# Optimization experiments

Measured on AMD Instinct MI355X. Metric: run time of the kernel, lower is better.

Reference implementation:

```python
import jax, jax.numpy as jnp
import numpy as np
from jax import lax

SEQ, B, IN, H, NLAYERS, OUT_LEN, OUT_SIZE = 80, 32768, 2, 10, 2, 20, 2


def _lstm_layer(x, h0, c0, Wih, Whh, bih, bhh):
    """PyTorch-convention LSTM layer. x: [T,B,F], h0/c0: [B,H]. Returns [T,B,H]."""
    b = bih + bhh  # [4H]

    def step(carry, xt):
        h, c = carry
        gates = xt @ Wih.T + h @ Whh.T + b  # [B,4H], gate order i,f,g,o
        i, f, g, o = jnp.split(gates, 4, axis=-1)
        i = jax.nn.sigmoid(i)
        f = jax.nn.sigmoid(f)
        g = jnp.tanh(g)
        o = jax.nn.sigmoid(o)
        c = f * c + i * g
        h = o * jnp.tanh(c)
        return (h, c), h

    (_, _), ys = lax.scan(step, (h0, c0), x)
    return ys


def setup_inputs() -> dict:
    key = jax.random.key(0)
    ks = jax.random.split(key, 16)
    s = 1.0 / np.sqrt(H)  # torch default init scale
    u = lambda k, shp: jax.random.uniform(k, shp, jnp.float32, -s, s)
    inp = {
        "x": jax.random.normal(ks[0], (SEQ, B, IN), jnp.float32),
        "h0": jnp.zeros((NLAYERS, B, H), jnp.float32),
        "c0": jnp.zeros((NLAYERS, B, H), jnp.float32),
        # layer 0 LSTM params
        "Wih0": u(ks[1], (4 * H, IN)),
        "Whh0": u(ks[2], (4 * H, H)),
        "bih0": u(ks[3], (4 * H,)),
        "bhh0": u(ks[4], (4 * H,)),
        # layer 1 LSTM params
        "Wih1": u(ks[5], (4 * H, H)),
        "Whh1": u(ks[6], (4 * H, H)),
        "bih1": u(ks[7], (4 * H,)),
        "bhh1": u(ks[8], (4 * H,)),
        # MLP head: Linear(800 -> 10), Sigmoid, Linear(10 -> 40)
        "W1": jax.random.uniform(ks[9], (H, SEQ * H), jnp.float32, -1 / np.sqrt(SEQ * H), 1 / np.sqrt(SEQ * H)),
        "b1": jax.random.uniform(ks[10], (H,), jnp.float32, -1 / np.sqrt(SEQ * H), 1 / np.sqrt(SEQ * H)),
        "W2": u(ks[11], (OUT_LEN * OUT_SIZE, H)),
        "b2": u(ks[12], (OUT_LEN * OUT_SIZE,)),
    }
    return inp


def reference(x, h0, c0, Wih0, Whh0, bih0, bhh0, Wih1, Whh1, bih1, bhh1, W1, b1, W2, b2):
    y0 = _lstm_layer(x, h0[0], c0[0], Wih0, Whh0, bih0, bhh0)   # [T,B,H]
    y1 = _lstm_layer(y0, h0[1], c0[1], Wih1, Whh1, bih1, bhh1)  # [T,B,H]
    out = jnp.tanh(y1)
    out = out.reshape(B, -1)  # faithful to torch .view(batch, -1) on [T,B,H]
    out = jax.nn.sigmoid(out @ W1.T + b1)
    out = out @ W2.T + b2  # [B, OUT_LEN*OUT_SIZE]
    return out.reshape(OUT_LEN, B, OUT_SIZE)
```

## Files before the change

kernel.cpp:

```cpp
#include <hip/hip_runtime.h>
#include <hip/hip_fp16.h>

#define SEQ   80
#define BATCH 32768
#define HID   10

typedef unsigned int uint;
typedef unsigned short ushort;
typedef _Float16 f16;
typedef __attribute__((ext_vector_type(8))) _Float16 f16x8;
typedef __attribute__((ext_vector_type(2))) _Float16 f16x2;
typedef __attribute__((ext_vector_type(4))) float f32x4;

#define SIG_SCALE  (-1.44269504f)
#define TANH_SCALE (-2.88539008f)

__device__ __forceinline__ float fast_rcp(float x)  { return __builtin_amdgcn_rcpf(x); }
__device__ __forceinline__ float fast_exp2(float x) { return __builtin_amdgcn_exp2f(x); }
__device__ __forceinline__ float sigp(float a)  { return fast_rcp(1.0f + fast_exp2(a)); }
__device__ __forceinline__ float tanhp(float a) { return 2.0f * fast_rcp(1.0f + fast_exp2(a)) - 1.0f; }
__device__ __forceinline__ float tanh_f(float x){ return tanhp(TANH_SCALE * x); }

union U4V { uint4 u; f16x8 v; };
union UH2 { uint u; f16x2 h; };
union HU  { f16 h; ushort s; };

__device__ __forceinline__ float lstm_unit(const f32x4 d, float& c) {
    const float Ei = fast_exp2(d[0]);
    const float Ef = fast_exp2(d[1]);
    const float Eg = fast_exp2(d[2]);
    const float Eo = fast_exp2(d[3]);
    const float Rf  = fast_rcp(1.0f + Ef);
    const float Rig = fast_rcp((1.0f + Ei) * (1.0f + Eg));
    c = c * Rf + (1.0f - Eg) * Rig;
    const float Ec = fast_exp2(TANH_SCALE * c);
    const float Rh = fast_rcp((1.0f + Eo) * (1.0f + Ec));
    return (1.0f - Ec) * Rh;
}

__global__ __launch_bounds__(256, 4)
void lstm2_spec(const float* __restrict__ x, const float* __restrict__ h0in,
                const float* __restrict__ c0in,
                const float* __restrict__ Wih0, const float* __restrict__ Whh0,
                const float* __restrict__ bih0, const float* __restrict__ bhh0,
                const float* __restrict__ Wih1, const float* __restrict__ Whh1,
                const float* __restrict__ bih1, const float* __restrict__ bhh1,
                ushort* __restrict__ y ) {
    __shared__ __align__(16) ushort buf[2][3][16][40];
    const int tid  = threadIdx.x;
    const int l    = tid & 63;
    const int wv   = tid >> 6;
    const int pair = wv >> 1;
    const int role = wv & 1;
    const int bl   = l & 15;
    const int grp  = l >> 4;
    const long b   = ((long)blockIdx.x * 2 + pair) * 16 + bl;

    f16x8 A[3];
    f32x4 bs[3];
#pragma unroll
    for (int T = 0; T < 3; ++T) {
        const int R  = 16 * T + bl;
        const int u  = R >> 2, gi = R & 3;
        const bool vr = (R < 40);
        const int tr = gi * 10 + u;
        const float sc = (gi == 2) ? TANH_SCALE : SIG_SCALE;
#pragma unroll
        for (int j = 0; j < 8; ++j) {
            const int k = grp * 8 + j;
            float w = 0.f;
            if (vr) {
                if (role == 0) {
                    if (k < 10)      w = Whh0[tr * 10 + k];
                    else if (k < 12) w = Wih0[tr * 2 + (k - 10)];
                } else {
                    if (k < 10)      w = Wih1[tr * 10 + k];
                    else if (k < 20) w = Whh1[tr * 10 + (k - 10)];
                }
            }
            A[T][j] = (f16)(w * sc);
        }
#pragma unroll
        for (int q = 0; q < 4; ++q) {
            const int Rc = 16 * T + grp * 4 + q;
            const int uc = Rc >> 2, gc = Rc & 3;
            const float scc = (gc == 2) ? TANH_SCALE : SIG_SCALE;
            const int trc = gc * 10 + uc;
            float bb = 0.f;
            if (Rc < 40)
                bb = (role == 0) ? (bih0[trc] + bhh0[trc]) : (bih1[trc] + bhh1[trc]);
            bs[T][q] = bb * scc;
        }
    }

    const size_t cbase = (role == 0) ? 0 : (size_t)BATCH * 10;
    float cS[3];
#pragma unroll
    for (int T = 0; T < 3; ++T) {
        const int u = 4 * T + grp;
        cS[T] = (u < 10) ? c0in[cbase + b * 10 + u] : 0.f;
    }

    {
        uint* p = (uint*)buf;
        for (int idx = tid; idx < 1920; idx += 256) p[idx] = 0u;
    }
    __syncthreads();
    if (role == 0) {
        ushort* row = &buf[pair][2][bl][0];
#pragma unroll
        for (int T = 0; T < 3; ++T) {
            const int u = 4 * T + grp;
            if (u < 10) { HU h; h.h = (f16)h0in[b * 10 + u]; row[u] = h.s; }
        }
    } else {
        ushort* row = &buf[pair][0][bl][0];
#pragma unroll
        for (int T = 0; T < 3; ++T) {
            const int u = 4 * T + grp;
            if (u < 10) { HU h; h.h = (f16)h0in[(size_t)BATCH * 10 + b * 10 + u]; row[10 + u] = h.s; }
        }
    }

    float2 xv = make_float2(0.f, 0.f);
    if (role == 0) xv = *reinterpret_cast<const float2*>(&x[b * 2]);

    for (int i = 0; i <= SEQ; ++i) {
        __syncthreads();
        const int wq = i % 3;
        const int rq = (i + 2) % 3;
        const ushort* rrow = &buf[pair][rq][bl][0];
        ushort* wrow = &buf[pair][wq][bl][0];

        if (role == 0) {
            if (i < SEQ) {
                const int tn = (i + 1 < SEQ) ? i + 1 : SEQ - 1;
                const float2 xnext = *reinterpret_cast<const float2*>(&x[((size_t)tn * BATCH + b) * 2]);

                U4V r; r.u = *reinterpret_cast<const uint4*>(rrow + grp * 8);
                UH2 xp; xp.h[0] = (f16)xv.x; xp.h[1] = (f16)xv.y;
                U4V bv;
                bv.u.x = (grp < 2)  ? r.u.x : 0u;
                bv.u.y = (grp == 0) ? r.u.y : ((grp == 1) ? xp.u : 0u);
                bv.u.z = (grp == 0) ? r.u.z : 0u;
                bv.u.w = (grp == 0) ? r.u.w : 0u;

                f32x4 d0 = __builtin_amdgcn_mfma_f32_16x16x32_f16(A[0], bv.v, bs[0], 0, 0, 0);
                f32x4 d1 = __builtin_amdgcn_mfma_f32_16x16x32_f16(A[1], bv.v, bs[1], 0, 0, 0);
                f32x4 d2 = __builtin_amdgcn_mfma_f32_16x16x32_f16(A[2], bv.v, bs[2], 0, 0, 0);

                HU hA; hA.h = (f16)lstm_unit(d0, cS[0]);
                HU hB; hB.h = (f16)lstm_unit(d1, cS[1]);
                HU hC; hC.h = (f16)lstm_unit(d2, cS[2]);

                wrow[grp] = hA.s;
                wrow[4 + grp] = hB.s;
                if (grp < 2) wrow[8 + grp] = hC.s;

                xv = xnext;
            }
        } else {
            if (i >= 1) {
                U4V r; r.u = *reinterpret_cast<const uint4*>(rrow + grp * 8);

                f32x4 d0 = __builtin_amdgcn_mfma_f32_16x16x32_f16(A[0], r.v, bs[0], 0, 0, 0);
                f32x4 d1 = __builtin_amdgcn_mfma_f32_16x16x32_f16(A[1], r.v, bs[1], 0, 0, 0);
                f32x4 d2 = __builtin_amdgcn_mfma_f32_16x16x32_f16(A[2], r.v, bs[2], 0, 0, 0);

                HU hA; hA.h = (f16)lstm_unit(d0, cS[0]);
                HU hB; hB.h = (f16)lstm_unit(d1, cS[1]);
                HU hC; hC.h = (f16)lstm_unit(d2, cS[2]);

                wrow[10 + grp] = hA.s;
                wrow[14 + grp] = hB.s;
                if (grp < 2) wrow[18 + grp] = hC.s;

                ushort* yp = y + (size_t)(i - 1) * BATCH * HID + b * HID;
                yp[grp] = hA.s;
                yp[4 + grp] = hB.s;
                if (grp < 2) yp[8 + grp] = hC.s;
            }
        }
    }
}

__global__ __launch_bounds__(256, 2)
void head_mfma(const ushort* __restrict__ yflat,
               const float* __restrict__ W1, const float* __restrict__ b1,
               const float* __restrict__ W2, const float* __restrict__ b2,
               float* __restrict__ out) {
    __shared__ float sbuf[4][16][12];
    const int tid = threadIdx.x;
    const int l   = tid & 63;
    const int wv  = tid >> 6;
    const int bl  = l & 15;
    const int grp = l >> 4;
    const long row = ((long)blockIdx.x * 4 + wv) * 16 + bl;

    const ushort* yrow = yflat + row * 800;
    const float* arow = W1 + (size_t)(bl < 10 ? bl : 9) * 800;

    f32x4 acc = {0.f, 0.f, 0.f, 0.f};
#pragma unroll 5
    for (int c = 0; c < 25; ++c) {
        U4V bv; bv.u = *reinterpret_cast<const uint4*>(yrow + c * 32 + grp * 8);
        f16x8 tv;
#pragma unroll
        for (int e = 0; e < 8; ++e)
            tv[e] = (f16)tanh_f((float)bv.v[e]);
        const float4 w0 = *reinterpret_cast<const float4*>(arow + c * 32 + grp * 8);
        const float4 w1 = *reinterpret_cast<const float4*>(arow + c * 32 + grp * 8 + 4);
        f16x8 af;
        af[0] = (f16)w0.x; af[1] = (f16)w0.y; af[2] = (f16)w0.z; af[3] = (f16)w0.w;
        af[4] = (f16)w1.x; af[5] = (f16)w1.y; af[6] = (f16)w1.z; af[7] = (f16)w1.w;
        acc = __builtin_amdgcn_mfma_f32_16x16x32_f16(af, tv, acc, 0, 0, 0);
    }

#pragma unroll
    for (int q = 0; q < 4; ++q) {
        const int o = grp * 4 + q;
        if (o < 10)
            sbuf[wv][bl][o] = sigp(SIG_SCALE * (acc[q] + b1[o]));
    }

    float s[10];
#pragma unroll
    for (int o = 0; o < 10; ++o) s[o] = sbuf[wv][bl][o];

    float* op = out + row * 40 + grp * 10;
#pragma unroll
    for (int jj = 0; jj < 10; ++jj) {
        const int j = grp * 10 + jj;
        float r = b2[j];
#pragma unroll
        for (int o = 0; o < 10; ++o) r += s[o] * W2[j * 10 + o];
        op[jj] = r;
    }
}

extern "C" void kernel_launch(void* const* d_in, const int* in_sizes, int n_in,
                              void* d_out, int out_size, void* d_ws, size_t ws_size,
                              hipStream_t stream) {
    const float* x    = (const float*)d_in[0];
    const float* h0   = (const float*)d_in[1];
    const float* c0   = (const float*)d_in[2];
    const float* Wih0 = (const float*)d_in[3];
    const float* Whh0 = (const float*)d_in[4];
    const float* bih0 = (const float*)d_in[5];
    const float* bhh0 = (const float*)d_in[6];
    const float* Wih1 = (const float*)d_in[7];
    const float* Whh1 = (const float*)d_in[8];
    const float* bih1 = (const float*)d_in[9];
    const float* bhh1 = (const float*)d_in[10];
    const float* W1   = (const float*)d_in[11];
    const float* b1   = (const float*)d_in[12];
    const float* W2   = (const float*)d_in[13];
    const float* b2   = (const float*)d_in[14];
    float* out = (float*)d_out;
    ushort* yws = (ushort*)d_ws;

    lstm2_spec<<<1024, 256, 0, stream>>>(x, h0, c0, Wih0, Whh0, bih0, bhh0,
                                         Wih1, Whh1, bih1, bhh1, yws);
    head_mfma<<<512, 256, 0, stream>>>(yws, W1, b1, W2, b2, out);
}
```

Before: 104.9 us.

## Shrink LSTM blocks to one wave pair, unroll ring buffer, share reciprocals

Each LSTM block now holds a single layer-0/layer-1 wave pair (128 threads, twice as many blocks). Each per-timestep __syncthreads therefore only couples two waves instead of four. The time loop is unrolled by three with fixed ring-buffer slots, which removes the modulo indexing and moves x/y addressing to pointer increments. The cell update now uses one combined reciprocal instead of two, packs x with cvt_pkrtz, and builds the MFMA operand with masks instead of selects. The cost is slightly different rounding in the gate math and a changed occupancy/register balance from the new launch bounds.

```diff
diff --git a/kernel.cpp b/kernel.cpp
--- a/kernel.cpp
+++ b/kernel.cpp
@@ -10,6 +10,7 @@
 typedef _Float16 f16;
 typedef __attribute__((ext_vector_type(8))) _Float16 f16x8;
 typedef __attribute__((ext_vector_type(2))) _Float16 f16x2;
+typedef __attribute__((ext_vector_type(2))) __fp16 fp16x2;
 typedef __attribute__((ext_vector_type(4))) float f32x4;
 
 #define SIG_SCALE  (-1.44269504f)
@@ -22,7 +23,7 @@
 __device__ __forceinline__ float tanh_f(float x){ return tanhp(TANH_SCALE * x); }
 
 union U4V { uint4 u; f16x8 v; };
-union UH2 { uint u; f16x2 h; };
+union UH2 { uint u; f16x2 h; fp16x2 p; };
 union HU  { f16 h; ushort s; };
 
 __device__ __forceinline__ float lstm_unit(const f32x4 d, float& c) {
@@ -30,15 +31,16 @@
     const float Ef = fast_exp2(d[1]);
     const float Eg = fast_exp2(d[2]);
     const float Eo = fast_exp2(d[3]);
-    const float Rf  = fast_rcp(1.0f + Ef);
-    const float Rig = fast_rcp((1.0f + Ei) * (1.0f + Eg));
-    c = c * Rf + (1.0f - Eg) * Rig;
+    const float Pi = 1.0f + Ei, Pf = 1.0f + Ef, Pg = 1.0f + Eg;
+    const float PiPg = Pi * Pg;
+    const float R = fast_rcp(PiPg * Pf);
+    c = c * (PiPg * R) + ((1.0f - Eg) * Pf) * R;
     const float Ec = fast_exp2(TANH_SCALE * c);
-    const float Rh = fast_rcp((1.0f + Eo) * (1.0f + Ec));
-    return (1.0f - Ec) * Rh;
-}
-
-__global__ __launch_bounds__(256, 4)
+    const float R2 = fast_rcp((1.0f + Eo) * (1.0f + Ec));
+    return (1.0f - Ec) * R2;
+}
+
+__global__ __launch_bounds__(128, 4)
 void lstm2_spec(const float* __restrict__ x, const float* __restrict__ h0in,
                 const float* __restrict__ c0in,
                 const float* __restrict__ Wih0, const float* __restrict__ Whh0,
@@ -46,15 +48,13 @@
                 const float* __restrict__ Wih1, const float* __restrict__ Whh1,
                 const float* __restrict__ bih1, const float* __restrict__ bhh1,
                 ushort* __restrict__ y ) {
-    __shared__ __align__(16) ushort buf[2][3][16][40];
+    __shared__ __align__(16) ushort buf[3][16][40];
     const int tid  = threadIdx.x;
     const int l    = tid & 63;
-    const int wv   = tid >> 6;
-    const int pair = wv >> 1;
-    const int role = wv & 1;
+    const int role = tid >> 6;
     const int bl   = l & 15;
     const int grp  = l >> 4;
-    const long b   = ((long)blockIdx.x * 2 + pair) * 16 + bl;
+    const long b   = (long)blockIdx.x * 16 + bl;
 
     f16x8 A[3];
     f32x4 bs[3];
@@ -103,18 +103,18 @@
 
     {
         uint* p = (uint*)buf;
-        for (int idx = tid; idx < 1920; idx += 256) p[idx] = 0u;
+        for (int idx = tid; idx < 960; idx += 128) p[idx] = 0u;
     }
     __syncthreads();
     if (role == 0) {
-        ushort* row = &buf[pair][2][bl][0];
+        ushort* row = &buf[2][bl][0];
 #pragma unroll
         for (int T = 0; T < 3; ++T) {
             const int u = 4 * T + grp;
             if (u < 10) { HU h; h.h = (f16)h0in[b * 10 + u]; row[u] = h.s; }
         }
     } else {
-        ushort* row = &buf[pair][0][bl][0];
+        ushort* row = &buf[0][bl][0];
 #pragma unroll
         for (int T = 0; T < 3; ++T) {
             const int u = 4 * T + grp;
@@ -122,65 +122,73 @@
         }
     }
 
+    const float* xq = x + b * 2 + (size_t)BATCH * 2;
     float2 xv = make_float2(0.f, 0.f);
-    if (role == 0) xv = *reinterpret_cast<const float2*>(&x[b * 2]);
-
-    for (int i = 0; i <= SEQ; ++i) {
+    if (role == 0) xv = *reinterpret_cast<const float2*>(x + b * 2);
+    ushort* yq = y + b * HID;
+
+    const uint mx  = (grp < 2)  ? 0xFFFFFFFFu : 0u;
+    const uint my0 = (grp == 0) ? 0xFFFFFFFFu : 0u;
+    const uint sx  = (grp == 1) ? 0xFFFFFFFFu : 0u;
+
+    auto body = [&](int i, ushort (*W)[40], const ushort (*Rb)[40]) {
         __syncthreads();
-        const int wq = i % 3;
-        const int rq = (i + 2) % 3;
-        const ushort* rrow = &buf[pair][rq][bl][0];
-        ushort* wrow = &buf[pair][wq][bl][0];
-
         if (role == 0) {
             if (i < SEQ) {
-                const int tn = (i + 1 < SEQ) ? i + 1 : SEQ - 1;
-                const float2 xnext = *reinterpret_cast<const float2*>(&x[((size_t)tn * BATCH + b) * 2]);
-
-                U4V r; r.u = *reinterpret_cast<const uint4*>(rrow + grp * 8);
-                UH2 xp; xp.h[0] = (f16)xv.x; xp.h[1] = (f16)xv.y;
+                const float2 xnext = *reinterpret_cast<const float2*>(xq);
+                U4V r; r.u = *reinterpret_cast<const uint4*>(&Rb[bl][0] + grp * 8);
+                UH2 xp; xp.p = __builtin_amdgcn_cvt_pkrtz(xv.x, xv.y);
                 U4V bv;
-                bv.u.x = (grp < 2)  ? r.u.x : 0u;
-                bv.u.y = (grp == 0) ? r.u.y : ((grp == 1) ? xp.u : 0u);
-                bv.u.z = (grp == 0) ? r.u.z : 0u;
-                bv.u.w = (grp == 0) ? r.u.w : 0u;
-
-                f32x4 d0 = __builtin_amdgcn_mfma_f32_16x16x32_f16(A[0], bv.v, bs[0], 0, 0, 0);
-                f32x4 d1 = __builtin_amdgcn_mfma_f32_16x16x32_f16(A[1], bv.v, bs[1], 0, 0, 0);
-                f32x4 d2 = __builtin_amdgcn_mfma_f32_16x16x32_f16(A[2], bv.v, bs[2], 0, 0, 0);
+                bv.u.x = r.u.x & mx;
+                bv.u.y = (r.u.y & my0) | (xp.u & sx);
+                bv.u.z = r.u.z & my0;
+                bv.u.w = r.u.w & my0;
+
+                const f32x4 d0 = __builtin_amdgcn_mfma_f32_16x16x32_f16(A[0], bv.v, bs[0], 0, 0, 0);
+                const f32x4 d1 = __builtin_amdgcn_mfma_f32_16x16x32_f16(A[1], bv.v, bs[1], 0, 0, 0);
+                const f32x4 d2 = __builtin_amdgcn_mfma_f32_16x16x32_f16(A[2], bv.v, bs[2], 0, 0, 0);
 
                 HU hA; hA.h = (f16)lstm_unit(d0, cS[0]);
                 HU hB; hB.h = (f16)lstm_unit(d1, cS[1]);
                 HU hC; hC.h = (f16)lstm_unit(d2, cS[2]);
 
-                wrow[grp] = hA.s;
+                ushort* wrow = &W[bl][0];
+                wrow[grp]     = hA.s;
                 wrow[4 + grp] = hB.s;
                 if (grp < 2) wrow[8 + grp] = hC.s;
 
                 xv = xnext;
+                if (i + 2 < SEQ) xq += (size_t)BATCH * 2;
             }
         } else {
             if (i >= 1) {
-                U4V r; r.u = *reinterpret_cast<const uint4*>(rrow + grp * 8);
-
-                f32x4 d0 = __builtin_amdgcn_mfma_f32_16x16x32_f16(A[0], r.v, bs[0], 0, 0, 0);
-                f32x4 d1 = __builtin_amdgcn_mfma_f32_16x16x32_f16(A[1], r.v, bs[1], 0, 0, 0);
-                f32x4 d2 = __builtin_amdgcn_mfma_f32_16x16x32_f16(A[2], r.v, bs[2], 0, 0, 0);
+                U4V r; r.u = *reinterpret_cast<const uint4*>(&Rb[bl][0] + grp * 8);
+
+                const f32x4 d0 = __builtin_amdgcn_mfma_f32_16x16x32_f16(A[0], r.v, bs[0], 0, 0, 0);
+                const f32x4 d1 = __builtin_amdgcn_mfma_f32_16x16x32_f16(A[1], r.v, bs[1], 0, 0, 0);
+                const f32x4 d2 = __builtin_amdgcn_mfma_f32_16x16x32_f16(A[2], r.v, bs[2], 0, 0, 0);
 
                 HU hA; hA.h = (f16)lstm_unit(d0, cS[0]);
                 HU hB; hB.h = (f16)lstm_unit(d1, cS[1]);
                 HU hC; hC.h = (f16)lstm_unit(d2, cS[2]);
 
+                ushort* wrow = &W[bl][0];
                 wrow[10 + grp] = hA.s;
                 wrow[14 + grp] = hB.s;
                 if (grp < 2) wrow[18 + grp] = hC.s;
 
-                ushort* yp = y + (size_t)(i - 1) * BATCH * HID + b * HID;
-                yp[grp] = hA.s;
-                yp[4 + grp] = hB.s;
-                if (grp < 2) yp[8 + grp] = hC.s;
+                yq[grp]     = hA.s;
+                yq[4 + grp] = hB.s;
+                if (grp < 2) yq[8 + grp] = hC.s;
+                yq += (size_t)BATCH * HID;
             }
         }
+    };
+
+    for (int i0 = 0; i0 < 81; i0 += 3) {
+        body(i0 + 0, buf[0], buf[2]);
+        body(i0 + 1, buf[1], buf[0]);
+        body(i0 + 2, buf[2], buf[1]);
     }
 }
 
@@ -259,7 +267,7 @@
     float* out = (float*)d_out;
     ushort* yws = (ushort*)d_ws;
 
-    lstm2_spec<<<1024, 256, 0, stream>>>(x, h0, c0, Wih0, Whh0, bih0, bhh0,
+    lstm2_spec<<<2048, 128, 0, stream>>>(x, h0, c0, Wih0, Whh0, bih0, bhh0,
                                          Wih1, Whh1, bih1, bhh1, yws);
     head_mfma<<<512, 256, 0, stream>>>(yws, W1, b1, W2, b2, out);
 }
```

Measured after the change: 102.3 us. 2.5% less time.
